# Kernel tuning notes

Hardware: AMD Instinct MI355X
Metric: run time of the kernel (lower is better)

The kernel has to match this reference:

```python
import jax, jax.numpy as jnp
import numpy as np

D, H, K = 384, 6, 8
B, NQ, NK = 4, 2048, 2048
EPS = 1e-5


def _ln(x, s, b):
    m = jnp.mean(x, axis=-1, keepdims=True)
    v = jnp.mean((x - m) ** 2, axis=-1, keepdims=True)
    return (x - m) * jax.lax.rsqrt(v + EPS) * s + b


def _mha(q, k, v, Wo, bo):
    # q,k,v: [B, N, D]
    dh = D // H
    qh = q.reshape(q.shape[0], q.shape[1], H, dh).transpose(0, 2, 1, 3)
    kh = k.reshape(k.shape[0], k.shape[1], H, dh).transpose(0, 2, 1, 3)
    vh = v.reshape(v.shape[0], v.shape[1], H, dh).transpose(0, 2, 1, 3)
    scores = jnp.einsum('bhqd,bhkd->bhqk', qh, kh) / jnp.sqrt(jnp.asarray(dh, q.dtype))
    attn = jax.nn.softmax(scores, axis=-1)
    out = jnp.einsum('bhqk,bhkd->bhqd', attn, vh)
    out = out.transpose(0, 2, 1, 3).reshape(q.shape[0], q.shape[1], D)
    return out @ Wo + bo


def _knn_edge(q_coords, k_coords, q_feats, k_feats):
    # coords: [B, N, 3]; feats: [B, N, D]. EdgeConv-style feature:
    # concat(neighbor_feat - center_feat, center_feat) -> [B, Nq, K, 2D]
    d2 = (jnp.sum(q_coords ** 2, -1)[:, :, None]
          + jnp.sum(k_coords ** 2, -1)[:, None, :]
          - 2.0 * jnp.einsum('bqc,bkc->bqk', q_coords, k_coords))
    _, idx = jax.lax.top_k(-d2, K)  # [B, Nq, K] nearest neighbors in key set
    neigh = jax.vmap(lambda f, i: f[i])(k_feats, idx)  # [B, Nq, K, D]
    center = jnp.broadcast_to(q_feats[:, :, None, :], neigh.shape)
    return jnp.concatenate([neigh - center, center], axis=-1)


def setup_inputs() -> dict:
    key = jax.random.key(0)
    ks = jax.random.split(key, 24)
    s = 0.02
    return {
        'query_points': jax.random.normal(ks[0], (B, 3 + D, NQ), jnp.float32),
        'key_points': jax.random.normal(ks[1], (B, 3 + D, NK), jnp.float32),
        'ln_in_s': jnp.ones((D,), jnp.float32), 'ln_in_b': jnp.zeros((D,), jnp.float32),
        'qkv_W': jax.random.normal(ks[2], (D, 3 * D), jnp.float32) * s,
        'attn_out_W': jax.random.normal(ks[3], (D, D), jnp.float32) * s,
        'attn_out_b': jnp.zeros((D,), jnp.float32),
        'ff_W1': jax.random.normal(ks[4], (D, 2 * D), jnp.float32) * s,
        'ff_b1': jnp.zeros((2 * D,), jnp.float32),
        'ff_W2': jax.random.normal(ks[5], (2 * D, D), jnp.float32) * s,
        'ff_b2': jnp.zeros((D,), jnp.float32),
        'ffn_s': jnp.ones((D,), jnp.float32), 'ffn_b': jnp.zeros((D,), jnp.float32),
        'knn1_W': jax.random.normal(ks[6], (2 * D, D), jnp.float32) * s,
        'knn1_b': jnp.zeros((D,), jnp.float32),
        'knn2_W': jax.random.normal(ks[7], (2 * D, D), jnp.float32) * s,
        'knn2_b': jnp.zeros((D,), jnp.float32),
        'self_merge_W': jax.random.normal(ks[8], (2 * D, D), jnp.float32) * s,
        'self_merge_b': jnp.zeros((D,), jnp.float32),
        'cross_merge_W': jax.random.normal(ks[9], (2 * D, D), jnp.float32) * s,
        'cross_merge_b': jnp.zeros((D,), jnp.float32),
        'cnq_s': jnp.ones((D,), jnp.float32), 'cnq_b': jnp.zeros((D,), jnp.float32),
        'cnk_s': jnp.ones((D,), jnp.float32), 'cnk_b': jnp.zeros((D,), jnp.float32),
        'cq_W': jax.random.normal(ks[10], (D, D), jnp.float32) * s,
        'ck_W': jax.random.normal(ks[11], (D, D), jnp.float32) * s,
        'cv_W': jax.random.normal(ks[12], (D, D), jnp.float32) * s,
    }


def reference(query_points, key_points, ln_in_s, ln_in_b, qkv_W, attn_out_W,
              attn_out_b, ff_W1, ff_b1, ff_W2, ff_b2, ffn_s, ffn_b,
              knn1_W, knn1_b, knn2_W, knn2_b, self_merge_W, self_merge_b,
              cross_merge_W, cross_merge_b, cnq_s, cnq_b, cnk_s, cnk_b,
              cq_W, ck_W, cv_W):
    qp = jnp.transpose(query_points, (0, 2, 1))  # [B, Nq, 3+D]
    kp = jnp.transpose(key_points, (0, 2, 1))    # [B, Nk, 3+D]
    q_coords, q_feats = qp[..., :3], qp[..., 3:]
    k_coords, k_feats = kp[..., :3], kp[..., 3:]

    # --- self attention + self kNN geometry ---
    norm_f = _ln(q_feats, ln_in_s, ln_in_b)
    qkv = norm_f @ qkv_W
    q, k, v = jnp.split(qkv, 3, axis=-1)
    attn_f = _mha(q, k, v, attn_out_W, attn_out_b)

    edge = _knn_edge(q_coords, q_coords, norm_f, norm_f)          # [B,Nq,K,2D]
    geom = jax.nn.leaky_relu(edge @ knn1_W + knn1_b, 0.2)
    geom = jnp.max(geom, axis=2)                                   # [B,Nq,D]

    attn_f = jnp.concatenate([attn_f, geom], axis=-1) @ self_merge_W + self_merge_b
    q_feats = attn_f + q_feats

    # --- cross attention + cross kNN geometry ---
    nq = _ln(q_feats, cnq_s, cnq_b)
    nk = _ln(k_feats, cnk_s, cnk_b)
    cross_f = _mha(nq @ cq_W, nk @ ck_W, nk @ cv_W, attn_out_W, attn_out_b)

    cedge = _knn_edge(q_coords, k_coords, nq, nk)                  # [B,Nq,K,2D]
    cgeom = jax.nn.leaky_relu(cedge @ knn2_W + knn2_b, 0.2)
    cgeom = jnp.max(cgeom, axis=2)

    cross_f = jnp.concatenate([cross_f, cgeom], axis=-1) @ cross_merge_W + cross_merge_b
    q_feats = q_feats + cross_f

    # --- feed forward ---
    h = _ln(q_feats, ffn_s, ffn_b)
    q_feats = q_feats + (jax.nn.gelu(h @ ff_W1 + ff_b1) @ ff_W2 + ff_b2)

    out = jnp.concatenate([q_coords, q_feats], axis=-1)
    return jnp.transpose(out, (0, 2, 1))  # [B, 3+D, Nq]
```

## Files before the change

kernel.cpp:

```cpp
#include <hip/hip_runtime.h>
#include <cstdint>
#include <cstddef>

#define NB 4
#define NN 2048
#define DD 384
#define NH 6

typedef float f4 __attribute__((ext_vector_type(4)));
typedef float f32x4 __attribute__((ext_vector_type(4)));
typedef short bf16x8 __attribute__((ext_vector_type(8)));
typedef unsigned u32x2 __attribute__((ext_vector_type(2)));

__device__ __forceinline__ float gelu_t(float x) {
  float x3 = x*x*x;
  return 0.5f*x*(1.0f + tanhf(0.7978845608028654f*(x + 0.044715f*x3)));
}

__device__ __forceinline__ unsigned short f2b(float f) {
  unsigned u = __builtin_bit_cast(unsigned, f);
  u += 0x7fffu + ((u >> 16) & 1u);
  return (unsigned short)(u >> 16);
}

__device__ __forceinline__ float b2f(unsigned short u) {
  return __builtin_bit_cast(float, ((unsigned)u) << 16);
}

__device__ __forceinline__ unsigned cvtpk(float a, float b) {
  unsigned r;
  asm("v_cvt_pk_bf16_f32 %0, %1, %2" : "=v"(r) : "v"(a), "v"(b));
  return r;
}

typedef __attribute__((address_space(1))) const void gvoid_t;
typedef __attribute__((address_space(3))) void lvoid_t;
__device__ __forceinline__ void gl16(const void* g, void* l) {
  __builtin_amdgcn_global_load_lds((gvoid_t*)g, (lvoid_t*)l, 16, 0, 0);
}

__device__ __forceinline__ unsigned long long shfl_xor_u64(unsigned long long v, int m) {
  unsigned lo = (unsigned)v, hi = (unsigned)(v >> 32);
  lo = (unsigned)__shfl_xor((int)lo, m);
  hi = (unsigned)__shfl_xor((int)hi, m);
  return ((unsigned long long)hi << 32) | lo;
}

__global__ __launch_bounds__(256) void split_k(const float* __restrict__ pts,
                                               float* __restrict__ coords,
                                               float* __restrict__ feats) {
  __shared__ float t[32][33];
  int b = blockIdx.z;
  int c0 = blockIdx.x*32, n0 = blockIdx.y*32;
  int tx = threadIdx.x, ty = threadIdx.y;
#pragma unroll
  for (int i = 0; i < 4; ++i) {
    int c = c0 + ty + i*8;
    if (c < 387) t[ty+i*8][tx] = pts[((size_t)b*387 + c)*NN + n0 + tx];
  }
  __syncthreads();
#pragma unroll
  for (int i = 0; i < 4; ++i) {
    int n = n0 + ty + i*8;
    int c = c0 + tx;
    if (c < 387) {
      float v = t[tx][ty+i*8];
      if (c < 3) coords[((size_t)b*NN + n)*4 + c] = v;
      else       feats[((size_t)b*NN + n)*DD + (c-3)] = v;
    }
    if (c0 == 0 && tx == 3) {
      float x = t[0][ty+i*8], y = t[1][ty+i*8], z = t[2][ty+i*8];
      coords[((size_t)b*NN + n)*4 + 3] = x*x + y*y + z*z;
    }
  }
}

__global__ __launch_bounds__(256) void pack_k(const float* __restrict__ coords,
                                              const float* __restrict__ feats,
                                              float* __restrict__ out) {
  __shared__ float t[32][33];
  int b = blockIdx.z;
  int c0 = blockIdx.x*32, n0 = blockIdx.y*32;
  int tx = threadIdx.x, ty = threadIdx.y;
#pragma unroll
  for (int i = 0; i < 4; ++i) {
    int n = n0 + ty + i*8;
    int c = c0 + tx;
    if (c < 387) {
      float v = (c < 3) ? coords[((size_t)b*NN + n)*4 + c]
                        : feats[((size_t)b*NN + n)*DD + (c-3)];
      t[tx][ty+i*8] = v;
    }
  }
  __syncthreads();
#pragma unroll
  for (int i = 0; i < 4; ++i) {
    int c = c0 + ty + i*8;
    if (c < 387) out[((size_t)b*387 + c)*NN + n0 + tx] = t[ty+i*8][tx];
  }
}

__device__ __forceinline__ void ln_body(const float* __restrict__ x,
                                        const float* __restrict__ g,
                                        const float* __restrict__ bb,
                                        unsigned short* __restrict__ o,
                                        int row) {
  int lane = threadIdx.x & 63;
  const float* xr = x + (size_t)row*DD;
  float v[6]; float s = 0.f;
#pragma unroll
  for (int i = 0; i < 6; ++i) { v[i] = xr[lane + i*64]; s += v[i]; }
#pragma unroll
  for (int off = 1; off < 64; off <<= 1) s += __shfl_xor(s, off);
  float mean = s * (1.f/384.f);
  float s2 = 0.f;
#pragma unroll
  for (int i = 0; i < 6; ++i) { float d = v[i] - mean; s2 += d*d; }
#pragma unroll
  for (int off = 1; off < 64; off <<= 1) s2 += __shfl_xor(s2, off);
  float rs = rsqrtf(s2*(1.f/384.f) + 1e-5f);
  unsigned short* orow = o + (size_t)row*DD;
#pragma unroll
  for (int i = 0; i < 6; ++i) {
    int c = lane + i*64;
    orow[c] = f2b((v[i]-mean)*rs*g[c] + bb[c]);
  }
}

__global__ __launch_bounds__(256) void ln_k(const float* __restrict__ x,
                                            const float* __restrict__ g,
                                            const float* __restrict__ bb,
                                            unsigned short* __restrict__ o) {
  ln_body(x, g, bb, o, blockIdx.x*4 + (threadIdx.x >> 6));
}

__global__ __launch_bounds__(256) void ln2_k(const float* __restrict__ x1,
                                             const float* __restrict__ g1,
                                             const float* __restrict__ b1,
                                             unsigned short* __restrict__ o1,
                                             const float* __restrict__ x2,
                                             const float* __restrict__ g2,
                                             const float* __restrict__ b2,
                                             unsigned short* __restrict__ o2) {
  int row = blockIdx.x*4 + (threadIdx.x >> 6);
  if (blockIdx.y == 0) ln_body(x1, g1, b1, o1, row);
  else                 ln_body(x2, g2, b2, o2, row);
}

struct WSrcs { const float* p[13]; };

__global__ __launch_bounds__(256) void wtrans_k(WSrcs srcs, unsigned short* __restrict__ dst) {
  constexpr int KK[13]  = {384,384,384,384,768,384,384,384,384,384,768,384,768};
  constexpr int NW[13]  = {1152,384,384,384,384,384,384,384,384,384,384,768,384};
  constexpr int MD[13]  = {0,0,2,0,0,0,0,0,0,2,0,0,0};
  constexpr int OFF[13] = {0,442368,589824,737280,884736,1179648,1327104,1474560,
                           1622016,1769472,1916928,2211840,2506752};
  constexpr int PFX[14] = {0,432,576,720,864,1152,1296,1440,1584,1728,1872,2160,2448,2736};
  int bid = blockIdx.x;
  int e = 0;
  while (bid >= PFX[e+1]) ++e;
  int t = bid - PFX[e];
  int K = KK[e], N = NW[e];
  int ntiles = N >> 5;
  int kt = t / ntiles, nt = t - kt*ntiles;
  const float* src = srcs.p[e];
  __shared__ float T[32][33];
  int tx = threadIdx.x & 31, ty = threadIdx.x >> 5;
  int n = nt*32 + tx;
#pragma unroll
  for (int i = 0; i < 4; ++i) {
    int k = kt*32 + ty + i*8;
    float v = src[(size_t)k*N + n];
    if (MD[e] == 2) v = src[(size_t)(k+384)*N + n] - v;
    T[ty+i*8][tx] = v;
  }
  __syncthreads();
#pragma unroll
  for (int i = 0; i < 4; ++i) {
    int nn = nt*32 + ty + i*8;
    int kk = kt*32 + tx;
    dst[(size_t)OFF[e] + (size_t)nn*K + kk] = f2b(T[tx][ty+i*8]);
  }
}

template<int ACT, int ACC, int OB, int HALFM>
__device__ __forceinline__ void mgemm_body(const unsigned short* __restrict__ A, int lda,
                                           const unsigned short* __restrict__ Wt,
                                           const float* __restrict__ bias,
                                           void* __restrict__ Cv, int ldc, int cofs,
                                           int Kd, int bx, int by, char* lds) {
  constexpr int BM   = HALFM ? 64 : 128;
  constexpr int MT   = HALFM ? 2 : 4;
  constexpr int AG   = HALFM ? 2 : 4;
  constexpr int ABUF = BM*128;
  constexpr int BUFSZ = ABUF + 8192;
  int tid = threadIdx.x;
  int lane = tid & 63, w = tid >> 6, g = lane >> 4, c = lane & 15;
  int wr = w >> 1, wc = w & 1;
  int m0 = by*BM, n0 = bx*64;
  int lrow = lane >> 3;
  int cswz = ((lane & 7) ^ lrow)*8;

  f32x4 acc[MT][2];
#pragma unroll
  for (int mt = 0; mt < MT; ++mt)
#pragma unroll
    for (int nt = 0; nt < 2; ++nt) acc[mt][nt] = 0.f;

  int KT = Kd >> 6;
  {
    char* As = lds; char* Bs = lds + ABUF;
#pragma unroll
    for (int i = 0; i < AG; ++i) {
      int rb = i*32 + w*8;
      gl16(A + (size_t)(m0 + rb + lrow)*lda + cswz, As + rb*128);
    }
#pragma unroll
    for (int i = 0; i < 2; ++i) {
      int rb = i*32 + w*8;
      gl16(Wt + (size_t)(n0 + rb + lrow)*Kd + cswz, Bs + rb*128);
    }
  }
  __syncthreads();

  for (int kt = 0; kt < KT; ++kt) {
    char* Asc = lds + (kt & 1)*BUFSZ;
    char* Bsc = Asc + ABUF;
    if (kt + 1 < KT) {
      char* Asn = lds + ((kt + 1) & 1)*BUFSZ;
      char* Bsn = Asn + ABUF;
      int k0 = (kt + 1)*64;
#pragma unroll
      for (int i = 0; i < AG; ++i) {
        int rb = i*32 + w*8;
        gl16(A + (size_t)(m0 + rb + lrow)*lda + k0 + cswz, Asn + rb*128);
      }
#pragma unroll
      for (int i = 0; i < 2; ++i) {
        int rb = i*32 + w*8;
        gl16(Wt + (size_t)(n0 + rb + lrow)*Kd + k0 + cswz, Bsn + rb*128);
      }
    }
#pragma unroll
    for (int kb = 0; kb < 2; ++kb) {
      bf16x8 af[MT], bfr[2];
#pragma unroll
      for (int mt = 0; mt < MT; ++mt) {
        int row = wr*(BM/2) + mt*16 + c;
        int ch = (kb*4 + g) ^ (row & 7);
        af[mt] = *(const bf16x8*)(Asc + row*128 + ch*16);
      }
#pragma unroll
      for (int nt = 0; nt < 2; ++nt) {
        int row = wc*32 + nt*16 + c;
        int ch = (kb*4 + g) ^ (row & 7);
        bfr[nt] = *(const bf16x8*)(Bsc + row*128 + ch*16);
      }
#pragma unroll
      for (int mt = 0; mt < MT; ++mt)
#pragma unroll
        for (int nt = 0; nt < 2; ++nt)
          acc[mt][nt] = __builtin_amdgcn_mfma_f32_16x16x32_bf16(af[mt], bfr[nt], acc[mt][nt], 0, 0, 0);
    }
    __syncthreads();
  }

#pragma unroll
  for (int mt = 0; mt < MT; ++mt) {
#pragma unroll
    for (int nt = 0; nt < 2; ++nt) {
      int coln = n0 + wc*32 + nt*16 + c;
      float bval = bias ? bias[coln] : 0.f;
#pragma unroll
      for (int r = 0; r < 4; ++r) {
        int m = m0 + wr*(BM/2) + mt*16 + 4*g + r;
        float t = acc[mt][nt][r] + bval;
        if (ACT == 1) t = gelu_t(t);
        if (OB) {
          ((unsigned short*)Cv)[(size_t)m*ldc + cofs + coln] = f2b(t);
        } else {
          float* cp = (float*)Cv + (size_t)m*ldc + cofs + coln;
          if (ACC) t += *cp;
          *cp = t;
        }
      }
    }
  }
}

template<int ACT, int ACC, int OB, int HALFM>
__global__ __launch_bounds__(256) void mgemm_k(const unsigned short* __restrict__ A, int lda,
                                               const unsigned short* __restrict__ Wt,
                                               const float* __restrict__ bias,
                                               void* __restrict__ Cv, int ldc, int cofs,
                                               int Kd) {
  constexpr int BM = HALFM ? 64 : 128;
  __shared__ char lds[2*(BM*128 + 8192)];
  mgemm_body<ACT,ACC,OB,HALFM>(A, lda, Wt, bias, Cv, ldc, cofs, Kd,
                               blockIdx.x, blockIdx.y, lds);
}

struct FSegs {
  const unsigned short* A[5];
  unsigned short* out[5];
  int ldc[5];
  int cofs[5];
};

__global__ __launch_bounds__(256) void fgemm_k(FSegs fs, const unsigned short* __restrict__ Wt) {
  __shared__ char lds[49152];
  int tid = threadIdx.x;
  int lane = tid & 63, w = tid >> 6, g = lane >> 4, c = lane & 15;
  int wr = w >> 1, wc = w & 1;
  int m0 = blockIdx.y*128, n0 = blockIdx.x*64;
  int seg = n0 / 384;
  const unsigned short* A = fs.A[seg];
  int lrow = lane >> 3;
  int cswz = ((lane & 7) ^ lrow)*8;

  f32x4 acc[4][2];
#pragma unroll
  for (int mt = 0; mt < 4; ++mt)
#pragma unroll
    for (int nt = 0; nt < 2; ++nt) acc[mt][nt] = 0.f;

  {
    char* As = lds; char* Bs = lds + 16384;
#pragma unroll
    for (int i = 0; i < 4; ++i) {
      int rb = i*32 + w*8;
      gl16(A + (size_t)(m0 + rb + lrow)*384 + cswz, As + rb*128);
    }
#pragma unroll
    for (int i = 0; i < 2; ++i) {
      int rb = i*32 + w*8;
      gl16(Wt + (size_t)(n0 + rb + lrow)*384 + cswz, Bs + rb*128);
    }
  }
  __syncthreads();

  for (int kt = 0; kt < 6; ++kt) {
    char* Asc = lds + (kt & 1)*24576;
    char* Bsc = Asc + 16384;
    if (kt + 1 < 6) {
      char* Asn = lds + ((kt + 1) & 1)*24576;
      char* Bsn = Asn + 16384;
      int k0 = (kt + 1)*64;
#pragma unroll
      for (int i = 0; i < 4; ++i) {
        int rb = i*32 + w*8;
        gl16(A + (size_t)(m0 + rb + lrow)*384 + k0 + cswz, Asn + rb*128);
      }
#pragma unroll
      for (int i = 0; i < 2; ++i) {
        int rb = i*32 + w*8;
        gl16(Wt + (size_t)(n0 + rb + lrow)*384 + k0 + cswz, Bsn + rb*128);
      }
    }
#pragma unroll
    for (int kb = 0; kb < 2; ++kb) {
      bf16x8 af[4], bfr[2];
#pragma unroll
      for (int mt = 0; mt < 4; ++mt) {
        int row = wr*64 + mt*16 + c;
        int ch = (kb*4 + g) ^ (row & 7);
        af[mt] = *(const bf16x8*)(Asc + row*128 + ch*16);
      }
#pragma unroll
      for (int nt = 0; nt < 2; ++nt) {
        int row = wc*32 + nt*16 + c;
        int ch = (kb*4 + g) ^ (row & 7);
        bfr[nt] = *(const bf16x8*)(Bsc + row*128 + ch*16);
      }
#pragma unroll
      for (int mt = 0; mt < 4; ++mt)
#pragma unroll
        for (int nt = 0; nt < 2; ++nt)
          acc[mt][nt] = __builtin_amdgcn_mfma_f32_16x16x32_bf16(af[mt], bfr[nt], acc[mt][nt], 0, 0, 0);
    }
    __syncthreads();
  }

  if (seg == 2) {
    unsigned short* vtp = fs.out[2];
    int bb = m0 >> 11;
    int tokb = (m0 & 2047) + wr*64 + 4*g;
#pragma unroll
    for (int mt = 0; mt < 4; ++mt) {
#pragma unroll
      for (int nt = 0; nt < 2; ++nt) {
        int cseg = (n0 - 768) + wc*32 + nt*16 + c;
        int h = cseg >> 6, d = cseg & 63;
        u32x2 pv;
        pv[0] = cvtpk(acc[mt][nt][0], acc[mt][nt][1]);
        pv[1] = cvtpk(acc[mt][nt][2], acc[mt][nt][3]);
        *(u32x2*)(vtp + ((size_t)((bb*NH + h)*64 + d))*NN + tokb + mt*16) = pv;
      }
    }
    return;
  }

  float qs = (seg == 0) ? 0.18033688011112042f : 1.0f;
  unsigned short* outp = fs.out[seg];
  int ldcs = fs.ldc[seg];
  int cbase = fs.cofs[seg] + (n0 - seg*384);
#pragma unroll
  for (int mt = 0; mt < 4; ++mt) {
#pragma unroll
    for (int nt = 0; nt < 2; ++nt) {
      int coln = cbase + wc*32 + nt*16 + c;
#pragma unroll
      for (int r = 0; r < 4; ++r) {
        int m = m0 + wr*64 + mt*16 + 4*g + r;
        outp[(size_t)m*ldcs + coln] = f2b(acc[mt][nt][r]*qs);
      }
    }
  }
}

__global__ __launch_bounds__(256) void flashm_k(const unsigned short* __restrict__ qkvb,
                                                const unsigned short* __restrict__ vt,
                                                unsigned short* __restrict__ o) {
  __shared__ char smem[40960];
  char* PT = smem + 32768;
  int bid = blockIdx.x;
  int s = (bid & 7)*96 + (bid >> 3);
  int qt = s & 31; int hb = s >> 5;
  int h = hb % NH, b = hb / NH;
  int q0 = qt*64;
  int tid = threadIdx.x;
  int w = tid >> 6, lane = tid & 63, g = lane >> 4, c = lane & 15;
  int lrow = lane >> 3;
  int gsw = ((lane & 7) ^ lrow)*8;

  const unsigned short* kbase = qkvb + (size_t)b*NN*1152 + 384 + h*64;
  const unsigned short* vbase = vt + ((size_t)(b*NH + h))*64*NN;

  bf16x8 qf[2];
  {
    const unsigned short* qrow = qkvb + ((size_t)(b*NN + q0 + w*16 + c))*1152 + h*64;
    qf[0] = *(const bf16x8*)(qrow + 8*g);
    qf[1] = *(const bf16x8*)(qrow + 32 + 8*g);
  }
  bf16x8 onesv;
#pragma unroll
  for (int i = 0; i < 8; ++i) onesv[i] = (short)0x3F80;

  f32x4 oacc[4];
#pragma unroll
  for (int i = 0; i < 4; ++i) oacc[i] = 0.f;
  f32x4 lacc = 0.f;

#define FSTAGE(bf, ktb) { \
    char* KB = smem + (bf)*16384; char* VB = KB + 8192; \
    gl16(kbase + (size_t)((ktb) + w*16 + lrow)*1152 + gsw,     KB + (w*16)*128); \
    gl16(kbase + (size_t)((ktb) + w*16 + 8 + lrow)*1152 + gsw, KB + (w*16+8)*128); \
    gl16(vbase + (size_t)(w*16 + lrow)*NN + (ktb) + gsw,       VB + (w*16)*128); \
    gl16(vbase + (size_t)(w*16 + 8 + lrow)*NN + (ktb) + gsw,   VB + (w*16+8)*128); }

  FSTAGE(0, 0);
  __syncthreads();

  for (int kt = 0; kt < 32; ++kt) {
    if (kt + 1 < 32) FSTAGE((kt + 1) & 1, (kt + 1)*64);
    char* KTc = smem + (kt & 1)*16384;
    char* VTc = KTc + 8192;

    f32x4 sT[4];
#pragma unroll
    for (int nt = 0; nt < 4; ++nt) sT[nt] = 0.f;
#pragma unroll
    for (int nt = 0; nt < 4; ++nt) {
      int krow = nt*16 + c;
#pragma unroll
      for (int kb = 0; kb < 2; ++kb) {
        int ch = ((kb*4 + g) ^ (krow & 7))*16;
        bf16x8 kf_ = *(const bf16x8*)(KTc + krow*128 + ch);
        sT[nt] = __builtin_amdgcn_mfma_f32_16x16x32_bf16(kf_, qf[kb], sT[nt], 0, 0, 0);
      }
    }

    int prow = w*16 + c;
    int pswz = (c & 7) << 4;
#pragma unroll
    for (int nt = 0; nt < 4; ++nt) {
      float p0 = __builtin_amdgcn_exp2f(sT[nt][0]);
      float p1 = __builtin_amdgcn_exp2f(sT[nt][1]);
      float p2 = __builtin_amdgcn_exp2f(sT[nt][2]);
      float p3 = __builtin_amdgcn_exp2f(sT[nt][3]);
      u32x2 pk;
      pk[0] = cvtpk(p0, p1);
      pk[1] = cvtpk(p2, p3);
      *(u32x2*)(PT + prow*128 + ((nt*32 + 8*g) ^ pswz)) = pk;
    }

    bf16x8 pb[2];
#pragma unroll
    for (int kb = 0; kb < 2; ++kb)
      pb[kb] = *(const bf16x8*)(PT + prow*128 + (((kb*4 + g) ^ (c & 7))*16));

    lacc = __builtin_amdgcn_mfma_f32_16x16x32_bf16(onesv, pb[0], lacc, 0, 0, 0);
    lacc = __builtin_amdgcn_mfma_f32_16x16x32_bf16(onesv, pb[1], lacc, 0, 0, 0);

#pragma unroll
    for (int dt = 0; dt < 4; ++dt) {
      int vrow = dt*16 + c;
#pragma unroll
      for (int kb = 0; kb < 2; ++kb) {
        int ch = ((kb*4 + g) ^ (vrow & 7))*16;
        bf16x8 vf = *(const bf16x8*)(VTc + vrow*128 + ch);
        oacc[dt] = __builtin_amdgcn_mfma_f32_16x16x32_bf16(vf, pb[kb], oacc[dt], 0, 0, 0);
      }
    }
    __syncthreads();
  }
#undef FSTAGE

  float inv = 1.f / lacc[0];
  size_t orow = ((size_t)b*NN + q0 + w*16 + c)*DD + h*64;
#pragma unroll
  for (int dt = 0; dt < 4; ++dt) {
    u32x2 ov;
    ov[0] = cvtpk(oacc[dt][0]*inv, oacc[dt][1]*inv);
    ov[1] = cvtpk(oacc[dt][2]*inv, oacc[dt][3]*inv);
    *(u32x2*)(o + orow + dt*16 + 4*g) = ov;
  }
}

__global__ __launch_bounds__(256) void knn2_k(const float* __restrict__ qc4,
                                              const float* __restrict__ kc4,
                                              int* __restrict__ idx1,
                                              int* __restrict__ idx2) {
  __shared__ unsigned long long sbuf[4][64];
  const float* kcs = blockIdx.y ? kc4 : qc4;
  int* idxo = blockIdx.y ? idx2 : idx1;
  int lane = threadIdx.x & 63;
  int w = threadIdx.x >> 6;
  int q = blockIdx.x*4 + w;
  int b = q >> 11;
  f4 qv = *(const f4*)(qc4 + (size_t)q*4);
  float mx_ = -2.f*qv[0], my_ = -2.f*qv[1], mz_ = -2.f*qv[2];
  const float* kb = kcs + (size_t)b*NN*4;

  float fv[32];
  float fm = INFINITY;
#pragma unroll
  for (int i = 0; i < 32; ++i) {
    f4 kv = *(const f4*)(kb + (size_t)(lane + i*64)*4);
    float f = fmaf(mx_, kv[0], fmaf(my_, kv[1], fmaf(mz_, kv[2], kv[3])));
    fv[i] = f;
    fm = fminf(fm, f);
  }

  {
    float v = fm;
#pragma unroll
    for (int k = 2; k <= 64; k <<= 1) {
#pragma unroll
      for (int j = k >> 1; j >= 1; j >>= 1) {
        float p = __shfl_xor(v, j);
        bool tmin = (((lane & k) == 0) == ((lane & j) == 0));
        v = tmin ? fminf(v, p) : fmaxf(v, p);
      }
    }
    fm = __shfl(v, 7);
  }
  float T = fm;

  int cnt = 0;
#pragma unroll
  for (int i = 0; i < 32; ++i) {
    bool p = fv[i] <= T;
    unsigned long long mask = __ballot(p);
    if (mask) {
      if (p) {
        int off = cnt + (int)__popcll(mask & ((1ull << lane) - 1ull));
        unsigned u = __builtin_bit_cast(unsigned, fv[i]);
        u ^= 0x80000000u | (unsigned)((int)u >> 31);
        if (off < 64)
          sbuf[w][off] = ((unsigned long long)u << 32) | (unsigned)(lane + i*64);
      }
      cnt += (int)__popcll(mask);
    }
  }

  unsigned long long key = ~0ull;
  if (lane < cnt && lane < 64) key = sbuf[w][lane];
#pragma unroll
  for (int k = 2; k <= 64; k <<= 1) {
#pragma unroll
    for (int j = k >> 1; j >= 1; j >>= 1) {
      unsigned long long p = shfl_xor_u64(key, j);
      bool tmin = (((lane & k) == 0) == ((lane & j) == 0));
      bool less = key < p;
      unsigned long long mn = less ? key : p;
      unsigned long long mx = less ? p : key;
      key = tmin ? mn : mx;
    }
  }
  if (lane < 8) idxo[(size_t)q*8 + lane] = (int)(unsigned)key;
}

__device__ __forceinline__ void geom_body(const unsigned short* __restrict__ GCb,
                                          const float* __restrict__ bias,
                                          const int* __restrict__ idx,
                                          unsigned short* __restrict__ out,
                                          int q) {
  int b = q >> 11;
  int t = threadIdx.x;
  int j[8];
#pragma unroll
  for (int k = 0; k < 8; ++k) j[k] = idx[(size_t)q*8 + k];
  const unsigned short* base = GCb + ((size_t)(b << 11))*768;
  {
    float c = b2f(GCb[(size_t)q*768 + 384 + t]) + bias[t];
    float mx = -INFINITY;
#pragma unroll
    for (int k = 0; k < 8; ++k) {
      float y = b2f(base[(size_t)j[k]*768 + t]) + c;
      y = (y > 0.f) ? y : 0.2f*y;
      mx = fmaxf(mx, y);
    }
    out[(size_t)q*768 + 384 + t] = f2b(mx);
  }
  if (t < 128) {
    int d = t + 256;
    float c = b2f(GCb[(size_t)q*768 + 384 + d]) + bias[d];
    float mx = -INFINITY;
#pragma unroll
    for (int k = 0; k < 8; ++k) {
      float y = b2f(base[(size_t)j[k]*768 + d]) + c;
      y = (y > 0.f) ? y : 0.2f*y;
      mx = fmaxf(mx, y);
    }
    out[(size_t)q*768 + 384 + d] = f2b(mx);
  }
}

__global__ __launch_bounds__(256) void wog_k(const unsigned short* __restrict__ A,
                                             const unsigned short* __restrict__ Wt,
                                             const float* __restrict__ wob,
                                             unsigned short* __restrict__ attnG,
                                             const unsigned short* __restrict__ GCb,
                                             const float* __restrict__ gbias,
                                             const int* __restrict__ idx) {
  __shared__ char lds[32768];
  int bid = blockIdx.x;
  int gq;
  if (bid < 8448) {
    int t = bid / 11, r = bid - t*11;
    if (r == 0) {
      mgemm_body<0,0,1,1>(A, 384, Wt, wob, attnG, 768, 0, 384, t % 6, t / 6, lds);
      return;
    }
    gq = t*10 + (r - 1);
  } else {
    gq = 7680 + (bid - 8448);
  }
  geom_body(GCb, gbias, idx, attnG, gq);
}

extern "C" void kernel_launch(void* const* d_in, const int* in_sizes, int n_in,
                              void* d_out, int out_size, void* d_ws, size_t ws_size,
                              hipStream_t stream) {
  (void)in_sizes; (void)n_in; (void)out_size; (void)ws_size;
  const float* qpts  = (const float*)d_in[0];
  const float* kpts  = (const float*)d_in[1];
  const float* ln_s  = (const float*)d_in[2];
  const float* ln_b  = (const float*)d_in[3];
  const float* qkvW  = (const float*)d_in[4];
  const float* Wo    = (const float*)d_in[5];
  const float* bo    = (const float*)d_in[6];
  const float* ffW1  = (const float*)d_in[7];
  const float* ffb1  = (const float*)d_in[8];
  const float* ffW2  = (const float*)d_in[9];
  const float* ffb2  = (const float*)d_in[10];
  const float* ffns  = (const float*)d_in[11];
  const float* ffnb  = (const float*)d_in[12];
  const float* knn1W = (const float*)d_in[13];
  const float* knn1b = (const float*)d_in[14];
  const float* knn2W = (const float*)d_in[15];
  const float* knn2b = (const float*)d_in[16];
  const float* smW   = (const float*)d_in[17];
  const float* smb   = (const float*)d_in[18];
  const float* cmW   = (const float*)d_in[19];
  const float* cmb   = (const float*)d_in[20];
  const float* cnqs  = (const float*)d_in[21];
  const float* cnqb  = (const float*)d_in[22];
  const float* cnks  = (const float*)d_in[23];
  const float* cnkb  = (const float*)d_in[24];
  const float* cqW   = (const float*)d_in[25];
  const float* ckW   = (const float*)d_in[26];
  const float* cvW   = (const float*)d_in[27];

  float* ws = (float*)d_ws;
  float* qc4  = ws;
  float* kc4  = qc4 + 32768;
  float* qf   = kc4 + 32768;
  float* kf   = qf + 3145728;
  unsigned short* nrmb = (unsigned short*)(kf + 3145728);
  unsigned short* nkb  = (unsigned short*)(kf + 3145728 + 1572864);
  float* qkv = kf + 3145728 + 1572864 + 1572864;
  unsigned short* qkvb   = (unsigned short*)qkv;
  unsigned short* attnGb = (unsigned short*)qkv;
  unsigned short* vtb    = (unsigned short*)(qkv + 4718592);
  unsigned short* wtb    = (unsigned short*)(qkv + 4718592 + 1572864);
  unsigned short* attnOb = (unsigned short*)(qkv + 4718592 + 1572864 + 1400832);
  unsigned short* GCbb   = (unsigned short*)((float*)attnOb + 1572864);
  int* idx1 = (int*)((float*)GCbb + 3145728);
  int* idx2 = idx1 + 65536;

  const int W_FA=0, W_WO=737280, W_SM=884736, W_FB=1179648,
            W_CM=1916928, W_FF1=2211840, W_FF2=2506752;

  WSrcs srcs;
  srcs.p[0]=qkvW; srcs.p[1]=knn1W; srcs.p[2]=knn1W; srcs.p[3]=Wo; srcs.p[4]=smW;
  srcs.p[5]=cqW; srcs.p[6]=ckW; srcs.p[7]=cvW; srcs.p[8]=knn2W; srcs.p[9]=knn2W;
  srcs.p[10]=cmW; srcs.p[11]=ffW1; srcs.p[12]=ffW2;
  wtrans_k<<<2736, 256, 0, stream>>>(srcs, wtb);

  dim3 tgrid(13, 64, NB), tblk(32, 8);
  split_k<<<tgrid, tblk, 0, stream>>>(qpts, qc4, qf);
  split_k<<<tgrid, tblk, 0, stream>>>(kpts, kc4, kf);

  knn2_k<<<dim3(2048, 2), 256, 0, stream>>>(qc4, kc4, idx1, idx2);

  dim3 mg384h(6, 128), mg768(12, 64), fg(30, 64);

  ln_k<<<2048, 256, 0, stream>>>(qf, ln_s, ln_b, nrmb);
  {
    FSegs fa;
    for (int s = 0; s < 5; ++s) fa.A[s] = nrmb;
    fa.out[0] = qkvb; fa.ldc[0] = 1152; fa.cofs[0] = 0;
    fa.out[1] = qkvb; fa.ldc[1] = 1152; fa.cofs[1] = 384;
    fa.out[2] = vtb;  fa.ldc[2] = 0;    fa.cofs[2] = 0;
    fa.out[3] = GCbb; fa.ldc[3] = 768;  fa.cofs[3] = 0;
    fa.out[4] = GCbb; fa.ldc[4] = 768;  fa.cofs[4] = 384;
    fgemm_k<<<fg, 256, 0, stream>>>(fa, wtb + W_FA);
  }
  flashm_k<<<768, 256, 0, stream>>>(qkvb, vtb, attnOb);
  wog_k<<<8960, 256, 0, stream>>>(attnOb, wtb+W_WO, bo, attnGb, GCbb, knn1b, idx1);
  mgemm_k<0,1,0,1><<<mg384h, 256, 0, stream>>>(attnGb, 768, wtb+W_SM, smb, qf, DD, 0, 768);

  ln2_k<<<dim3(2048, 2), 256, 0, stream>>>(qf, cnqs, cnqb, nrmb, kf, cnks, cnkb, nkb);
  {
    FSegs fb;
    fb.A[0] = nrmb; fb.A[1] = nkb; fb.A[2] = nkb; fb.A[3] = nkb; fb.A[4] = nrmb;
    fb.out[0] = qkvb; fb.ldc[0] = 1152; fb.cofs[0] = 0;
    fb.out[1] = qkvb; fb.ldc[1] = 1152; fb.cofs[1] = 384;
    fb.out[2] = vtb;  fb.ldc[2] = 0;    fb.cofs[2] = 0;
    fb.out[3] = GCbb; fb.ldc[3] = 768;  fb.cofs[3] = 0;
    fb.out[4] = GCbb; fb.ldc[4] = 768;  fb.cofs[4] = 384;
    fgemm_k<<<fg, 256, 0, stream>>>(fb, wtb + W_FB);
  }
  flashm_k<<<768, 256, 0, stream>>>(qkvb, vtb, attnOb);
  wog_k<<<8960, 256, 0, stream>>>(attnOb, wtb+W_WO, bo, attnGb, GCbb, knn2b, idx2);
  mgemm_k<0,1,0,1><<<mg384h, 256, 0, stream>>>(attnGb, 768, wtb+W_CM, cmb, qf, DD, 0, 768);

  ln_k<<<2048, 256, 0, stream>>>(qf, ffns, ffnb, nrmb);
  mgemm_k<1,0,1,0><<<mg768, 256, 0, stream>>>(nrmb, DD, wtb+W_FF1, ffb1, attnGb, 768, 0, DD);
  mgemm_k<0,1,0,1><<<mg384h, 256, 0, stream>>>(attnGb, 768, wtb+W_FF2, ffb2, qf, DD, 0, 768);

  pack_k<<<tgrid, tblk, 0, stream>>>(qc4, qf, (float*)d_out);
}
```

Before: 309.8 us.

## Split flash attention over two KV halves with a separate combine kernel

The attention kernel now divides the 2048 keys into two halves, so twice as many blocks run, each doing half the KV loop. Each block writes unnormalised fp32 partial outputs and row sums to a workspace. A new combine kernel adds the two partials, normalises, and writes bf16. This raises parallelism and shortens each block's serial loop, at the cost of an extra launch and a large fp32 partial round-trip through memory. That round-trip is about 25 MB per attention call.

```diff
diff --git a/kernel.cpp b/kernel.cpp
--- a/kernel.cpp
+++ b/kernel.cpp
@@ -420,12 +420,13 @@
 
 __global__ __launch_bounds__(256) void flashm_k(const unsigned short* __restrict__ qkvb,
                                                 const unsigned short* __restrict__ vt,
-                                                unsigned short* __restrict__ o) {
+                                                float* __restrict__ pO,
+                                                float* __restrict__ pL) {
   __shared__ char smem[40960];
   char* PT = smem + 32768;
   int bid = blockIdx.x;
-  int s = (bid & 7)*96 + (bid >> 3);
-  int qt = s & 31; int hb = s >> 5;
+  int s = (bid & 7)*192 + (bid >> 3);
+  int qt = s & 31, sp = (s >> 5) & 1, hb = s >> 6;
   int h = hb % NH, b = hb / NH;
   int q0 = qt*64;
   int tid = threadIdx.x;
@@ -453,17 +454,18 @@
 
 #define FSTAGE(bf, ktb) { \
     char* KB = smem + (bf)*16384; char* VB = KB + 8192; \
-    gl16(kbase + (size_t)((ktb) + w*16 + lrow)*1152 + gsw,     KB + (w*16)*128); \
-    gl16(kbase + (size_t)((ktb) + w*16 + 8 + lrow)*1152 + gsw, KB + (w*16+8)*128); \
-    gl16(vbase + (size_t)(w*16 + lrow)*NN + (ktb) + gsw,       VB + (w*16)*128); \
-    gl16(vbase + (size_t)(w*16 + 8 + lrow)*NN + (ktb) + gsw,   VB + (w*16+8)*128); }
-
-  FSTAGE(0, 0);
+    gl16(kbase + (size_t)((ktb)*64 + w*16 + lrow)*1152 + gsw,     KB + (w*16)*128); \
+    gl16(kbase + (size_t)((ktb)*64 + w*16 + 8 + lrow)*1152 + gsw, KB + (w*16+8)*128); \
+    gl16(vbase + (size_t)(w*16 + lrow)*NN + (ktb)*64 + gsw,       VB + (w*16)*128); \
+    gl16(vbase + (size_t)(w*16 + 8 + lrow)*NN + (ktb)*64 + gsw,   VB + (w*16+8)*128); }
+
+  int kt0 = sp*16;
+  FSTAGE(0, kt0);
   __syncthreads();
 
-  for (int kt = 0; kt < 32; ++kt) {
-    if (kt + 1 < 32) FSTAGE((kt + 1) & 1, (kt + 1)*64);
-    char* KTc = smem + (kt & 1)*16384;
+  for (int t2 = 0; t2 < 16; ++t2) {
+    if (t2 + 1 < 16) FSTAGE((t2 + 1) & 1, kt0 + t2 + 1);
+    char* KTc = smem + (t2 & 1)*16384;
     char* VTc = KTc + 8192;
 
     f32x4 sT[4];
@@ -516,14 +518,37 @@
   }
 #undef FSTAGE
 
-  float inv = 1.f / lacc[0];
-  size_t orow = ((size_t)b*NN + q0 + w*16 + c)*DD + h*64;
-#pragma unroll
-  for (int dt = 0; dt < 4; ++dt) {
+  int blk = (hb*32 + qt)*2 + sp;
+  float* po = pO + (size_t)blk*4096;
+  int q = w*16 + c;
+#pragma unroll
+  for (int dt = 0; dt < 4; ++dt)
+    *(f4*)(po + q*64 + dt*16 + 4*g) = oacc[dt];
+  if (g == 0) pL[(size_t)blk*64 + q] = lacc[0];
+}
+
+__global__ __launch_bounds__(256) void comb_k(const float* __restrict__ pO,
+                                              const float* __restrict__ pL,
+                                              unsigned short* __restrict__ o) {
+  int blk = blockIdx.x;
+  int hb = blk >> 5, qt = blk & 31;
+  int h = hb % NH, b = hb / NH;
+  const float* p0 = pO + (size_t)blk*2*4096;
+  const float* p1 = p0 + 4096;
+  const float* l0 = pL + (size_t)blk*2*64;
+  int t = threadIdx.x;
+  int q = t >> 2, d0 = (t & 3)*16;
+  float inv = 1.f / (l0[q] + l0[64 + q]);
+  size_t orow = ((size_t)b*NN + qt*64 + q)*DD + h*64 + d0;
+#pragma unroll
+  for (int i = 0; i < 16; i += 4) {
+    f4 a = *(const f4*)(p0 + q*64 + d0 + i);
+    f4 bb = *(const f4*)(p1 + q*64 + d0 + i);
+    a = (a + bb)*inv;
     u32x2 ov;
-    ov[0] = cvtpk(oacc[dt][0]*inv, oacc[dt][1]*inv);
-    ov[1] = cvtpk(oacc[dt][2]*inv, oacc[dt][3]*inv);
-    *(u32x2*)(o + orow + dt*16 + 4*g) = ov;
+    ov[0] = cvtpk(a[0], a[1]);
+    ov[1] = cvtpk(a[2], a[3]);
+    *(u32x2*)(o + orow + i) = ov;
   }
 }
 
@@ -709,6 +734,8 @@
   unsigned short* GCbb   = (unsigned short*)((float*)attnOb + 1572864);
   int* idx1 = (int*)((float*)GCbb + 3145728);
   int* idx2 = idx1 + 65536;
+  float* pO = (float*)(idx2 + 65536);
+  float* pL = pO + 6291456;
 
   const int W_FA=0, W_WO=737280, W_SM=884736, W_FB=1179648,
             W_CM=1916928, W_FF1=2211840, W_FF2=2506752;
@@ -738,7 +765,8 @@
     fa.out[4] = GCbb; fa.ldc[4] = 768;  fa.cofs[4] = 384;
     fgemm_k<<<fg, 256, 0, stream>>>(fa, wtb + W_FA);
   }
-  flashm_k<<<768, 256, 0, stream>>>(qkvb, vtb, attnOb);
+  flashm_k<<<1536, 256, 0, stream>>>(qkvb, vtb, pO, pL);
+  comb_k<<<768, 256, 0, stream>>>(pO, pL, attnOb);
   wog_k<<<8960, 256, 0, stream>>>(attnOb, wtb+W_WO, bo, attnGb, GCbb, knn1b, idx1);
   mgemm_k<0,1,0,1><<<mg384h, 256, 0, stream>>>(attnGb, 768, wtb+W_SM, smb, qf, DD, 0, 768);
 
@@ -753,7 +781,8 @@
     fb.out[4] = GCbb; fb.ldc[4] = 768;  fb.cofs[4] = 384;
     fgemm_k<<<fg, 256, 0, stream>>>(fb, wtb + W_FB);
   }
-  flashm_k<<<768, 256, 0, stream>>>(qkvb, vtb, attnOb);
+  flashm_k<<<1536, 256, 0, stream>>>(qkvb, vtb, pO, pL);
+  comb_k<<<768, 256, 0, stream>>>(pO, pL, attnOb);
   wog_k<<<8960, 256, 0, stream>>>(attnOb, wtb+W_WO, bo, attnGb, GCbb, knn2b, idx2);
   mgemm_k<0,1,0,1><<<mg384h, 256, 0, stream>>>(attnGb, 768, wtb+W_CM, cmb, qf, DD, 0, 768);
 
```

New measurement: 321.8 us. 3.9% more time.
